# Kernel tuning notes

Measured on AMD Instinct MI355X. Metric: run time of the kernel, lower is better.

The kernel has to match this reference:

```python
import math
import jax, jax.numpy as jnp
import numpy as np

N = 512; E_EDGES = 16384; NODE_DIM = 64; HID = 128; FF = 2048; VOCAB = 50; L = 2; H = 8; SEQ = 100


def setup_inputs() -> dict:
    key = jax.random.key(0)
    ks = jax.random.split(key, 24)
    s = 0.02
    rn = lambda k, shape: jax.random.normal(k, shape, jnp.float32) * s
    return {
        "x": jax.random.normal(ks[0], (N, NODE_DIM), jnp.float32),
        "edge_index": jax.random.randint(ks[1], (2, E_EDGES), 0, N, dtype=jnp.int32),
        "gcn1_w": rn(ks[2], (NODE_DIM, HID)), "gcn1_b": rn(ks[3], (HID,)),
        "gcn2_w": rn(ks[4], (HID, HID)),     "gcn2_b": rn(ks[5], (HID,)),
        "fc_w":   rn(ks[6], (HID, HID)),     "fc_b":   rn(ks[7], (HID,)),
        # decoder: per layer, 4 proj mats (q,k,v,out) for self-attn and cross-attn
        "sa_w": rn(ks[8], (L, 4, HID, HID)), "sa_b": rn(ks[9], (L, 4, HID)),
        "ca_w": rn(ks[10], (L, 4, HID, HID)), "ca_b": rn(ks[11], (L, 4, HID)),
        "ln_w": jnp.ones((L, 3, HID), jnp.float32), "ln_b": jnp.zeros((L, 3, HID), jnp.float32),
        "ff_w1": rn(ks[12], (L, HID, FF)), "ff_b1": rn(ks[13], (L, FF)),
        "ff_w2": rn(ks[14], (L, FF, HID)), "ff_b2": rn(ks[15], (L, HID)),
        "out_w": rn(ks[16], (HID, VOCAB)), "out_b": rn(ks[17], (VOCAB,)),
    }


def _gcn(x, W, b, src, dst, n):
    # PyG GCNConv: add self-loops, symmetric norm, aggregate source->target
    h = x @ W                                   # [N, out]
    loop = jnp.arange(n, dtype=src.dtype)
    s = jnp.concatenate([src, loop])
    d = jnp.concatenate([dst, loop])
    deg = jax.ops.segment_sum(jnp.ones_like(d, x.dtype), d, num_segments=n)
    dinv = jax.lax.rsqrt(deg)                   # deg >= 1 thanks to self-loops
    norm = dinv[s] * dinv[d]                    # [E+N]
    return jax.ops.segment_sum(h[s] * norm[:, None], d, num_segments=n) + b


def _layernorm(x, w, b, eps=1e-5):
    m = x.mean(-1, keepdims=True)
    v = ((x - m) ** 2).mean(-1, keepdims=True)
    return (x - m) * jax.lax.rsqrt(v + eps) * w + b


def _mha(q_in, kv_in, w, b):
    # q_in [S,Nb,E], kv_in [T,Nb,E]; w [4,E,E] (q,k,v,out), b [4,E]
    S, Nb, E = q_in.shape
    T = kv_in.shape[0]
    Dh = E // H
    q = (q_in @ w[0] + b[0]).reshape(S, Nb, H, Dh)
    k = (kv_in @ w[1] + b[1]).reshape(T, Nb, H, Dh)
    v = (kv_in @ w[2] + b[2]).reshape(T, Nb, H, Dh)
    att = jnp.einsum('snhd,tnhd->nhst', q, k) / math.sqrt(Dh)
    p = jax.nn.softmax(att, axis=-1)
    o = jnp.einsum('nhst,tnhd->snhd', p, v).reshape(S, Nb, E)
    return o @ w[3] + b[3]


def _forward(x, edge_index, gcn1_w, gcn1_b, gcn2_w, gcn2_b, fc_w, fc_b,
             sa_w, sa_b, ca_w, ca_b, ln_w, ln_b, ff_w1, ff_b1, ff_w2, ff_b2,
             out_w, out_b):
    n = x.shape[0]
    src, dst = edge_index[0], edge_index[1]
    # quantum_embedding: rz = (cos(phi)-sin(phi)) * (cos(theta)*x + sin(theta)*tanh(x))
    qx = (math.cos(0.05) - math.sin(0.05)) * (math.cos(0.1) * x + math.sin(0.1) * jnp.tanh(x))
    h = jax.nn.relu(_gcn(qx, gcn1_w, gcn1_b, src, dst, n))
    h = jax.nn.relu(_gcn(h, gcn2_w, gcn2_b, src, dst, n))
    h = h @ fc_w + fc_b                          # [N, HID]
    mem = h[None]                                # [1, N, HID] (memory, seq-first)
    tgt = jnp.zeros((SEQ, n, h.shape[1]), h.dtype)
    for l in range(L):                           # post-norm TransformerDecoderLayer
        tgt = _layernorm(tgt + _mha(tgt, tgt, sa_w[l], sa_b[l]), ln_w[l, 0], ln_b[l, 0])
        tgt = _layernorm(tgt + _mha(tgt, mem, ca_w[l], ca_b[l]), ln_w[l, 1], ln_b[l, 1])
        f = jax.nn.relu(tgt @ ff_w1[l] + ff_b1[l]) @ ff_w2[l] + ff_b2[l]
        tgt = _layernorm(tgt + f, ln_w[l, 2], ln_b[l, 2])
    return tgt @ out_w + out_b                   # [SEQ, N, VOCAB]


def reference(x, edge_index, gcn1_w, gcn1_b, gcn2_w, gcn2_b, fc_w, fc_b,
              sa_w, sa_b, ca_w, ca_b, ln_w, ln_b, ff_w1, ff_b1, ff_w2, ff_b2,
              out_w, out_b):
    return _forward(x, edge_index, gcn1_w, gcn1_b, gcn2_w, gcn2_b, fc_w, fc_b,
                    sa_w, sa_b, ca_w, ca_b, ln_w, ln_b, ff_w1, ff_b1, ff_w2, ff_b2,
                    out_w, out_b)
```

## Files before the change

### kernel.cpp

```cpp
#include <hip/hip_runtime.h>
#include <math.h>

#define NN      512
#define EE      16384
#define NDIM    64
#define HID     128
#define FFD     2048
#define VOCAB   50
#define SEQ     100

#define QA 0.94877109112428797f
#define QB 0.99500416527802582f
#define QC 0.099833416646828155f

struct GArgs {
    const int* ei;
    const float* x; const float* g1w; const float* g1b;
    const float* g2w; const float* g2b;
    const float* fcw; const float* fcb;
    const float* saw; const float* sab;
    const float* caw; const float* cab;
    const float* lnw; const float* lnb;
    const float* fw1; const float* fb1; const float* fw2; const float* fb2;
    const float* ow; const float* ob;
    float* out;
    int* offs; int* csr;
    float* dinv; float* pre1; float* pre2; float* t2;
    float* Msa1; float* Mca0; float* Mca1; float* sa0bias;
};


__device__ __forceinline__ float gather_row(const float* __restrict__ pre,
                                            const float* __restrict__ dinv,
                                            const int* __restrict__ offs,
                                            const int* __restrict__ csr,
                                            int row, int j) {
    float dd = dinv[row];
    float acc = pre[row * HID + j] * dd;
    int i = offs[row], e = offs[row + 1];
    for (; i + 3 < e; i += 4) {
        int s0 = csr[i], s1 = csr[i + 1], s2 = csr[i + 2], s3 = csr[i + 3];
        float a0 = pre[s0 * HID + j] * dinv[s0];
        float a1 = pre[s1 * HID + j] * dinv[s1];
        float a2 = pre[s2 * HID + j] * dinv[s2];
        float a3 = pre[s3 * HID + j] * dinv[s3];
        acc += (a0 + a1) + (a2 + a3);
    }
    for (; i < e; ++i) {
        int s = csr[i];
        acc += pre[s * HID + j] * dinv[s];
    }
    return acc * dd;
}

__device__ __forceinline__ float rowln4(float v, float w, float b, float* sh, int t) {
    int r = t >> 7;
    float s1 = v, s2 = v * v;
#pragma unroll
    for (int o = 32; o > 0; o >>= 1) {
        s1 += __shfl_down(s1, o);
        s2 += __shfl_down(s2, o);
    }
    int wv = (t >> 6) & 1;
    if ((t & 63) == 0) { sh[r * 4 + wv] = s1; sh[r * 4 + 2 + wv] = s2; }
    __syncthreads();
    float mean = (sh[r * 4] + sh[r * 4 + 1]) * (1.0f / HID);
    float m2   = (sh[r * 4 + 2] + sh[r * 4 + 3]) * (1.0f / HID);
    float rstd = rsqrtf(m2 - mean * mean + 1e-5f);
    float out = (v - mean) * rstd * w + b;
    __syncthreads();
    return out;
}

__device__ __forceinline__ float ff_core(const float* __restrict__ W1,
                                         const float* __restrict__ b1,
                                         const float* __restrict__ W2,
                                         const float* sh_x, float* sh_m, int t) {
    {
        int c4 = t * 4;
        float4 bb = *(const float4*)&b1[c4];
        float a0x = bb.x, a0y = bb.y, a0z = bb.z, a0w = bb.w;
        float a1x = bb.x, a1y = bb.y, a1z = bb.z, a1w = bb.w;
        float a2x = bb.x, a2y = bb.y, a2z = bb.z, a2w = bb.w;
        float a3x = bb.x, a3y = bb.y, a3z = bb.z, a3w = bb.w;
        const float* w1p = W1 + c4;
#pragma unroll 4
        for (int k = 0; k < HID; k++) {
            float4 w = *(const float4*)&w1p[k * FFD];
            float s0 = sh_x[0 * HID + k], s1 = sh_x[1 * HID + k];
            float s2 = sh_x[2 * HID + k], s3 = sh_x[3 * HID + k];
            a0x = fmaf(s0, w.x, a0x); a0y = fmaf(s0, w.y, a0y);
            a0z = fmaf(s0, w.z, a0z); a0w = fmaf(s0, w.w, a0w);
            a1x = fmaf(s1, w.x, a1x); a1y = fmaf(s1, w.y, a1y);
            a1z = fmaf(s1, w.z, a1z); a1w = fmaf(s1, w.w, a1w);
            a2x = fmaf(s2, w.x, a2x); a2y = fmaf(s2, w.y, a2y);
            a2z = fmaf(s2, w.z, a2z); a2w = fmaf(s2, w.w, a2w);
            a3x = fmaf(s3, w.x, a3x); a3y = fmaf(s3, w.y, a3y);
            a3z = fmaf(s3, w.z, a3z); a3w = fmaf(s3, w.w, a3w);
        }
        float4 m;
        m.x = fmaxf(a0x, 0.f); m.y = fmaxf(a0y, 0.f); m.z = fmaxf(a0z, 0.f); m.w = fmaxf(a0w, 0.f);
        *(float4*)&sh_m[0 * FFD + c4] = m;
        m.x = fmaxf(a1x, 0.f); m.y = fmaxf(a1y, 0.f); m.z = fmaxf(a1z, 0.f); m.w = fmaxf(a1w, 0.f);
        *(float4*)&sh_m[1 * FFD + c4] = m;
        m.x = fmaxf(a2x, 0.f); m.y = fmaxf(a2y, 0.f); m.z = fmaxf(a2z, 0.f); m.w = fmaxf(a2w, 0.f);
        *(float4*)&sh_m[2 * FFD + c4] = m;
        m.x = fmaxf(a3x, 0.f); m.y = fmaxf(a3y, 0.f); m.z = fmaxf(a3z, 0.f); m.w = fmaxf(a3w, 0.f);
        *(float4*)&sh_m[3 * FFD + c4] = m;
    }
    __syncthreads();

    float4 p0 = {0, 0, 0, 0}, p1 = p0, p2 = p0, p3 = p0;
    {
        int col4 = (t & 31) * 4, k0 = (t >> 5) * 128;
        const float* w2p = W2 + col4;
#pragma unroll 8
        for (int kk = 0; kk < 128; kk++) {
            int k = k0 + kk;
            float4 w = *(const float4*)&w2p[k * HID];
            float m0 = sh_m[0 * FFD + k], m1 = sh_m[1 * FFD + k];
            float m2 = sh_m[2 * FFD + k], m3 = sh_m[3 * FFD + k];
            p0.x = fmaf(m0, w.x, p0.x); p0.y = fmaf(m0, w.y, p0.y);
            p0.z = fmaf(m0, w.z, p0.z); p0.w = fmaf(m0, w.w, p0.w);
            p1.x = fmaf(m1, w.x, p1.x); p1.y = fmaf(m1, w.y, p1.y);
            p1.z = fmaf(m1, w.z, p1.z); p1.w = fmaf(m1, w.w, p1.w);
            p2.x = fmaf(m2, w.x, p2.x); p2.y = fmaf(m2, w.y, p2.y);
            p2.z = fmaf(m2, w.z, p2.z); p2.w = fmaf(m2, w.w, p2.w);
            p3.x = fmaf(m3, w.x, p3.x); p3.y = fmaf(m3, w.y, p3.y);
            p3.z = fmaf(m3, w.z, p3.z); p3.w = fmaf(m3, w.w, p3.w);
        }
    }
    __syncthreads();
    {
        int col4 = (t & 31) * 4, kq = t >> 5;
        *(float4*)&sh_m[kq * 512 + 0 * 128 + col4] = p0;
        *(float4*)&sh_m[kq * 512 + 1 * 128 + col4] = p1;
        *(float4*)&sh_m[kq * 512 + 2 * 128 + col4] = p2;
        *(float4*)&sh_m[kq * 512 + 3 * 128 + col4] = p3;
    }
    __syncthreads();
    int j = t & 127, r = t >> 7;
    float v = 0.0f;
#pragma unroll
    for (int kq = 0; kq < 16; kq++) v += sh_m[kq * 512 + r * 128 + j];
    return v;
}


__global__ __launch_bounds__(512) void k_a(GArgs a) {
    __shared__ __align__(16) float smem[1024];
    int bid = blockIdx.x, t = threadIdx.x;
    if (bid == 0) {
        int* scnt = (int*)smem;
        int* scur = scnt + 512;
        scnt[t] = 0;
        __syncthreads();
#pragma unroll
        for (int i = 0; i < 32; i++) {
            int e = i * 512 + t;
            atomicAdd(&scnt[a.ei[EE + e]], 1);
        }
        __syncthreads();
        int c = scnt[t];
        int v = c;
        for (int o = 1; o < 512; o <<= 1) {
            int add = (t >= o) ? scnt[t - o] : 0;
            __syncthreads();
            v += add;
            scnt[t] = v;
            __syncthreads();
        }
        a.offs[t + 1] = v;
        if (t == 0) a.offs[0] = 0;
        scur[t] = v - c;
        a.dinv[t] = rsqrtf((float)c + 1.0f);
        __syncthreads();
#pragma unroll
        for (int i = 0; i < 32; i++) {
            int e = i * 512 + t;
            int d = a.ei[EE + e];
            int slot = atomicAdd(&scur[d], 1);
            a.csr[slot] = a.ei[e];
        }
    } else if (bid <= 64) {
        float* qxs = smem;
        int row0 = (bid - 1) * 8;
        float vx = a.x[row0 * NDIM + t];
        qxs[t] = QA * (QB * vx + QC * tanhf(vx));
        __syncthreads();
        int col = t & 127, r0 = t >> 7;
#pragma unroll
        for (int rr = 0; rr < 2; rr++) {
            int r = r0 + rr * 4;
            float acc = 0.0f;
#pragma unroll 8
            for (int k = 0; k < NDIM; k++)
                acc = fmaf(qxs[r * 64 + k], a.g1w[k * HID + col], acc);
            a.pre1[(row0 + r) * HID + col] = acc;
        }
    } else if (bid <= 163) {
        int q = bid - 65;
        int jm = q / 33;
        int i = (q - jm * 33) * 512 + t;
        if (i < 129 * HID) {
            const float* A  = (jm == 0) ? (a.saw + (4 + 2) * HID * HID)
                             : (jm == 1) ? (a.caw + 2 * HID * HID)
                                         : (a.caw + (4 + 2) * HID * HID);
            const float* ab = (jm == 0) ? (a.sab + (4 + 2) * HID)
                             : (jm == 1) ? (a.cab + 2 * HID)
                                         : (a.cab + (4 + 2) * HID);
            const float* Bm = (jm == 0) ? (a.saw + (4 + 3) * HID * HID)
                             : (jm == 1) ? (a.caw + 3 * HID * HID)
                                         : (a.caw + (4 + 3) * HID * HID);
            const float* bb = (jm == 0) ? (a.sab + (4 + 3) * HID)
                             : (jm == 1) ? (a.cab + 3 * HID)
                                         : (a.cab + (4 + 3) * HID);
            float* outM = (jm == 0) ? a.Msa1 : (jm == 1) ? a.Mca0 : a.Mca1;
            int rw = i >> 7, col = i & 127;
            float acc;
            if (rw < 128) {
                const float* ar = A + rw * HID;
                acc = 0.0f;
#pragma unroll 8
                for (int k = 0; k < HID; k++) acc = fmaf(ar[k], Bm[k * HID + col], acc);
            } else {
                acc = bb[col];
#pragma unroll 8
                for (int k = 0; k < HID; k++) acc = fmaf(ab[k], Bm[k * HID + col], acc);
            }
            outM[i] = acc;
        }
    } else {
        if (t < HID) {
            const float* ab3 = a.sab + 2 * HID;
            const float* B3  = a.saw + 3 * HID * HID;
            float acc = a.sab[3 * HID + t];
#pragma unroll 8
            for (int k = 0; k < HID; k++) acc = fmaf(ab3[k], B3[k * HID + t], acc);
            a.sa0bias[t] = acc;
        }
    }
}


__global__ __launch_bounds__(512) void k_b2(GArgs a) {
    __shared__ float sh_h[4 * HID];
    int t = threadIdx.x, j = t & 127, r = t >> 7;
    int row = blockIdx.x * 4 + r;
    float g = gather_row(a.pre1, a.dinv, a.offs, a.csr, row, j);
    sh_h[r * HID + j] = fmaxf(g + a.g1b[j], 0.0f);
    __syncthreads();
    float acc = 0.0f;
#pragma unroll 8
    for (int k = 0; k < HID; k++)
        acc = fmaf(sh_h[r * HID + k], a.g2w[k * HID + j], acc);
    a.pre2[row * HID + j] = acc;
}


__global__ __launch_bounds__(512) void k_ffA(GArgs a) {
    __shared__ __align__(16) float sh_x[4 * HID];
    __shared__ __align__(16) float sh_h[4 * HID];
    __shared__ __align__(16) float sh_ca[4 * HID];
    __shared__ __align__(16) float sh_m[4 * FFD];
    __shared__ float shln[16];
    int bid = blockIdx.x, t = threadIdx.x;
    int j = t & 127, r = t >> 7;
    int row = bid * 4 + r;

    float g = gather_row(a.pre2, a.dinv, a.offs, a.csr, row, j);
    sh_h[r * HID + j] = fmaxf(g + a.g2b[j], 0.0f);
    __syncthreads();
    float mv = a.fcb[j];
#pragma unroll 8
    for (int k = 0; k < HID; k++) mv = fmaf(sh_h[r * HID + k], a.fcw[k * HID + j], mv);
    __syncthreads();
    sh_h[r * HID + j] = mv;
    __syncthreads();
    float c0 = a.Mca0[128 * HID + j], c1 = a.Mca1[128 * HID + j];
#pragma unroll 4
    for (int k = 0; k < HID; k++) {
        float m = sh_h[r * HID + k];
        c0 = fmaf(m, a.Mca0[k * HID + j], c0);
        c1 = fmaf(m, a.Mca1[k * HID + j], c1);
    }
    sh_ca[r * HID + j] = c1;
    float v0 = rowln4(a.sa0bias[j], a.lnw[j], a.lnb[j], shln, t);
    v0 = rowln4(v0 + c0, a.lnw[HID + j], a.lnb[HID + j], shln, t);
    sh_x[r * HID + j] = v0;
    __syncthreads();

    float v = ff_core(a.fw1, a.fb1, a.fw2, sh_x, sh_m, t);

    v += a.fb2[j] + sh_x[r * HID + j];
    float t1 = rowln4(v, a.lnw[2 * HID + j], a.lnb[2 * HID + j], shln, t);
    __syncthreads();
    sh_h[r * HID + j] = t1;
    __syncthreads();
    float s1 = a.Msa1[128 * HID + j];
#pragma unroll 8
    for (int k = 0; k < HID; k++)
        s1 = fmaf(sh_h[r * HID + k], a.Msa1[k * HID + j], s1);
    float u = rowln4(t1 + s1, a.lnw[3 * HID + j], a.lnb[3 * HID + j], shln, t);
    u = rowln4(u + sh_ca[r * HID + j], a.lnw[4 * HID + j], a.lnb[4 * HID + j], shln, t);
    a.t2[row * HID + j] = u;
}


__global__ __launch_bounds__(512) void k_ffB(GArgs a) {
    __shared__ __align__(16) float sh_x[4 * HID];
    __shared__ __align__(16) float sh_h[4 * HID];
    __shared__ __align__(16) float sh_m[4 * FFD];
    __shared__ __align__(16) float sh_lg[4 * VOCAB];
    __shared__ float shln[16];
    int bid = blockIdx.x, t = threadIdx.x;
    int j = t & 127, r = t >> 7;

    if (t < 128) ((float4*)sh_x)[t] = ((const float4*)(a.t2 + bid * 4 * HID))[t];
    __syncthreads();

    float v = ff_core(a.fw1 + HID * FFD, a.fb1 + FFD, a.fw2 + FFD * HID, sh_x, sh_m, t);

    v += a.fb2[HID + j] + sh_x[r * HID + j];
    float w = rowln4(v, a.lnw[5 * HID + j], a.lnb[5 * HID + j], shln, t);
    __syncthreads();
    sh_h[r * HID + j] = w;
    __syncthreads();
    if (t < 4 * VOCAB) {
        int rr = t / VOCAB, c = t - rr * VOCAB;
        float acc = a.ob[c];
#pragma unroll 8
        for (int k = 0; k < HID; k++)
            acc = fmaf(sh_h[rr * HID + k], a.ow[k * VOCAB + c], acc);
        sh_lg[rr * VOCAB + c] = acc;
    }
    __syncthreads();
    const float4* lg4 = (const float4*)sh_lg;
    float4* out4 = (float4*)a.out;
    int base4 = bid * 50;
    for (int idx = t; idx < SEQ * 50; idx += 512) {
        int s = idx / 50, q = idx - s * 50;
        out4[s * (NN * VOCAB / 4) + base4 + q] = lg4[q];
    }
}


extern "C" void kernel_launch(void* const* d_in, const int* in_sizes, int n_in,
                              void* d_out, int out_size, void* d_ws, size_t ws_size,
                              hipStream_t stream) {
    (void)in_sizes; (void)n_in; (void)out_size; (void)ws_size;
    GArgs a;
    a.x   = (const float*)d_in[0];
    a.ei  = (const int*)d_in[1];
    a.g1w = (const float*)d_in[2];
    a.g1b = (const float*)d_in[3];
    a.g2w = (const float*)d_in[4];
    a.g2b = (const float*)d_in[5];
    a.fcw = (const float*)d_in[6];
    a.fcb = (const float*)d_in[7];
    a.saw = (const float*)d_in[8];
    a.sab = (const float*)d_in[9];
    a.caw = (const float*)d_in[10];
    a.cab = (const float*)d_in[11];
    a.lnw = (const float*)d_in[12];
    a.lnb = (const float*)d_in[13];
    a.fw1 = (const float*)d_in[14];
    a.fb1 = (const float*)d_in[15];
    a.fw2 = (const float*)d_in[16];
    a.fb2 = (const float*)d_in[17];
    a.ow  = (const float*)d_in[18];
    a.ob  = (const float*)d_in[19];
    a.out = (float*)d_out;

    float* ws = (float*)d_ws;
    a.pre1    = ws;
    a.pre2    = ws + 65536;
    a.t2      = ws + 131072;
    a.Msa1    = ws + 196608;
    a.Mca0    = ws + 213120;
    a.Mca1    = ws + 229632;
    a.sa0bias = ws + 246144;
    a.dinv    = ws + 246272;
    a.offs    = (int*)(ws + 246784);
    a.csr     = a.offs + 516;

    k_a  <<<165, 512, 0, stream>>>(a);
    k_b2 <<<128, 512, 0, stream>>>(a);
    k_ffA<<<128, 512, 0, stream>>>(a);
    k_ffB<<<128, 512, 0, stream>>>(a);
}
```

Before: 123.1 us.

## Split FF kernels to two rows per block and stagger weight reads

```diff
diff --git a/kernel.cpp b/kernel.cpp
--- a/kernel.cpp
+++ b/kernel.cpp
@@ -25,7 +25,7 @@
     const float* ow; const float* ob;
     float* out;
     int* offs; int* csr;
-    float* dinv; float* pre1; float* pre2; float* t2;
+    float* dinv; float* pre1; float* pre2; float* t0; float* ca1; float* t2;
     float* Msa1; float* Mca0; float* Mca1; float* sa0bias;
 };
 
@@ -72,77 +72,60 @@
     return out;
 }
 
-__device__ __forceinline__ float ff_core(const float* __restrict__ W1,
-                                         const float* __restrict__ b1,
-                                         const float* __restrict__ W2,
-                                         const float* sh_x, float* sh_m, int t) {
+__device__ __forceinline__ float ff2_core(const float* __restrict__ W1,
+                                          const float* __restrict__ b1,
+                                          const float* __restrict__ W2,
+                                          const float* sh_x, float* sh_m,
+                                          float* sh_p, int t, int koff) {
     {
         int c4 = t * 4;
         float4 bb = *(const float4*)&b1[c4];
         float a0x = bb.x, a0y = bb.y, a0z = bb.z, a0w = bb.w;
         float a1x = bb.x, a1y = bb.y, a1z = bb.z, a1w = bb.w;
-        float a2x = bb.x, a2y = bb.y, a2z = bb.z, a2w = bb.w;
-        float a3x = bb.x, a3y = bb.y, a3z = bb.z, a3w = bb.w;
         const float* w1p = W1 + c4;
-#pragma unroll 4
-        for (int k = 0; k < HID; k++) {
+#pragma unroll 8
+        for (int kk = 0; kk < HID; kk++) {
+            int k = (kk + koff) & (HID - 1);
             float4 w = *(const float4*)&w1p[k * FFD];
-            float s0 = sh_x[0 * HID + k], s1 = sh_x[1 * HID + k];
-            float s2 = sh_x[2 * HID + k], s3 = sh_x[3 * HID + k];
+            float s0 = sh_x[k], s1 = sh_x[HID + k];
             a0x = fmaf(s0, w.x, a0x); a0y = fmaf(s0, w.y, a0y);
             a0z = fmaf(s0, w.z, a0z); a0w = fmaf(s0, w.w, a0w);
             a1x = fmaf(s1, w.x, a1x); a1y = fmaf(s1, w.y, a1y);
             a1z = fmaf(s1, w.z, a1z); a1w = fmaf(s1, w.w, a1w);
-            a2x = fmaf(s2, w.x, a2x); a2y = fmaf(s2, w.y, a2y);
-            a2z = fmaf(s2, w.z, a2z); a2w = fmaf(s2, w.w, a2w);
-            a3x = fmaf(s3, w.x, a3x); a3y = fmaf(s3, w.y, a3y);
-            a3z = fmaf(s3, w.z, a3z); a3w = fmaf(s3, w.w, a3w);
         }
         float4 m;
-        m.x = fmaxf(a0x, 0.f); m.y = fmaxf(a0y, 0.f); m.z = fmaxf(a0z, 0.f); m.w = fmaxf(a0w, 0.f);
-        *(float4*)&sh_m[0 * FFD + c4] = m;
-        m.x = fmaxf(a1x, 0.f); m.y = fmaxf(a1y, 0.f); m.z = fmaxf(a1z, 0.f); m.w = fmaxf(a1w, 0.f);
-        *(float4*)&sh_m[1 * FFD + c4] = m;
-        m.x = fmaxf(a2x, 0.f); m.y = fmaxf(a2y, 0.f); m.z = fmaxf(a2z, 0.f); m.w = fmaxf(a2w, 0.f);
-        *(float4*)&sh_m[2 * FFD + c4] = m;
-        m.x = fmaxf(a3x, 0.f); m.y = fmaxf(a3y, 0.f); m.z = fmaxf(a3z, 0.f); m.w = fmaxf(a3w, 0.f);
-        *(float4*)&sh_m[3 * FFD + c4] = m;
-    }
-    __syncthreads();
-
-    float4 p0 = {0, 0, 0, 0}, p1 = p0, p2 = p0, p3 = p0;
+        m.x = fmaxf(a0x, 0.f); m.y = fmaxf(a0y, 0.f);
+        m.z = fmaxf(a0z, 0.f); m.w = fmaxf(a0w, 0.f);
+        *(float4*)&sh_m[c4] = m;
+        m.x = fmaxf(a1x, 0.f); m.y = fmaxf(a1y, 0.f);
+        m.z = fmaxf(a1z, 0.f); m.w = fmaxf(a1w, 0.f);
+        *(float4*)&sh_m[FFD + c4] = m;
+    }
+    __syncthreads();
+
     {
-        int col4 = (t & 31) * 4, k0 = (t >> 5) * 128;
+        int kq = t >> 5, col4 = (t & 31) * 4;
+        int k0 = kq * 128;
+        float4 p0 = {0, 0, 0, 0}, p1 = {0, 0, 0, 0};
         const float* w2p = W2 + col4;
 #pragma unroll 8
         for (int kk = 0; kk < 128; kk++) {
-            int k = k0 + kk;
+            int k = k0 + ((kk + koff) & 127);
             float4 w = *(const float4*)&w2p[k * HID];
-            float m0 = sh_m[0 * FFD + k], m1 = sh_m[1 * FFD + k];
-            float m2 = sh_m[2 * FFD + k], m3 = sh_m[3 * FFD + k];
+            float m0 = sh_m[k], m1 = sh_m[FFD + k];
             p0.x = fmaf(m0, w.x, p0.x); p0.y = fmaf(m0, w.y, p0.y);
             p0.z = fmaf(m0, w.z, p0.z); p0.w = fmaf(m0, w.w, p0.w);
             p1.x = fmaf(m1, w.x, p1.x); p1.y = fmaf(m1, w.y, p1.y);
             p1.z = fmaf(m1, w.z, p1.z); p1.w = fmaf(m1, w.w, p1.w);
-            p2.x = fmaf(m2, w.x, p2.x); p2.y = fmaf(m2, w.y, p2.y);
-            p2.z = fmaf(m2, w.z, p2.z); p2.w = fmaf(m2, w.w, p2.w);
-            p3.x = fmaf(m3, w.x, p3.x); p3.y = fmaf(m3, w.y, p3.y);
-            p3.z = fmaf(m3, w.z, p3.z); p3.w = fmaf(m3, w.w, p3.w);
-        }
-    }
-    __syncthreads();
-    {
-        int col4 = (t & 31) * 4, kq = t >> 5;
-        *(float4*)&sh_m[kq * 512 + 0 * 128 + col4] = p0;
-        *(float4*)&sh_m[kq * 512 + 1 * 128 + col4] = p1;
-        *(float4*)&sh_m[kq * 512 + 2 * 128 + col4] = p2;
-        *(float4*)&sh_m[kq * 512 + 3 * 128 + col4] = p3;
-    }
-    __syncthreads();
-    int j = t & 127, r = t >> 7;
+        }
+        *(float4*)&sh_p[kq * 256 + col4] = p0;
+        *(float4*)&sh_p[kq * 256 + 128 + col4] = p1;
+    }
+    __syncthreads();
+    int j = t & 127, r = (t >> 7) & 1;
     float v = 0.0f;
 #pragma unroll
-    for (int kq = 0; kq < 16; kq++) v += sh_m[kq * 512 + r * 128 + j];
+    for (int kq = 0; kq < 16; kq++) v += sh_p[kq * 256 + r * 128 + j];
     return v;
 }
 
@@ -258,16 +241,13 @@
 }
 
 
-__global__ __launch_bounds__(512) void k_ffA(GArgs a) {
-    __shared__ __align__(16) float sh_x[4 * HID];
-    __shared__ __align__(16) float sh_h[4 * HID];
-    __shared__ __align__(16) float sh_ca[4 * HID];
-    __shared__ __align__(16) float sh_m[4 * FFD];
-    __shared__ float shln[16];
-    int bid = blockIdx.x, t = threadIdx.x;
-    int j = t & 127, r = t >> 7;
-    int row = bid * 4 + r;
-
+__global__ __launch_bounds__(512) void k_c2(GArgs a) {
+    __shared__ __align__(16) float smem[1040];
+    float* sh_h = smem;
+    float* sh_m = smem + 512;
+    float* shln = smem + 1024;
+    int t = threadIdx.x, j = t & 127, r = t >> 7;
+    int row = blockIdx.x * 4 + r;
     float g = gather_row(a.pre2, a.dinv, a.offs, a.csr, row, j);
     sh_h[r * HID + j] = fmaxf(g + a.g2b[j], 0.0f);
     __syncthreads();
@@ -275,71 +255,85 @@
 #pragma unroll 8
     for (int k = 0; k < HID; k++) mv = fmaf(sh_h[r * HID + k], a.fcw[k * HID + j], mv);
     __syncthreads();
-    sh_h[r * HID + j] = mv;
+    sh_m[r * HID + j] = mv;
     __syncthreads();
     float c0 = a.Mca0[128 * HID + j], c1 = a.Mca1[128 * HID + j];
 #pragma unroll 4
     for (int k = 0; k < HID; k++) {
-        float m = sh_h[r * HID + k];
+        float m = sh_m[r * HID + k];
         c0 = fmaf(m, a.Mca0[k * HID + j], c0);
         c1 = fmaf(m, a.Mca1[k * HID + j], c1);
     }
-    sh_ca[r * HID + j] = c1;
-    float v0 = rowln4(a.sa0bias[j], a.lnw[j], a.lnb[j], shln, t);
-    v0 = rowln4(v0 + c0, a.lnw[HID + j], a.lnb[HID + j], shln, t);
-    sh_x[r * HID + j] = v0;
-    __syncthreads();
-
-    float v = ff_core(a.fw1, a.fb1, a.fw2, sh_x, sh_m, t);
-
-    v += a.fb2[j] + sh_x[r * HID + j];
-    float t1 = rowln4(v, a.lnw[2 * HID + j], a.lnb[2 * HID + j], shln, t);
-    __syncthreads();
-    sh_h[r * HID + j] = t1;
-    __syncthreads();
-    float s1 = a.Msa1[128 * HID + j];
-#pragma unroll 8
-    for (int k = 0; k < HID; k++)
-        s1 = fmaf(sh_h[r * HID + k], a.Msa1[k * HID + j], s1);
-    float u = rowln4(t1 + s1, a.lnw[3 * HID + j], a.lnb[3 * HID + j], shln, t);
-    u = rowln4(u + sh_ca[r * HID + j], a.lnw[4 * HID + j], a.lnb[4 * HID + j], shln, t);
-    a.t2[row * HID + j] = u;
-}
-
-
-__global__ __launch_bounds__(512) void k_ffB(GArgs a) {
-    __shared__ __align__(16) float sh_x[4 * HID];
-    __shared__ __align__(16) float sh_h[4 * HID];
-    __shared__ __align__(16) float sh_m[4 * FFD];
-    __shared__ __align__(16) float sh_lg[4 * VOCAB];
+    a.ca1[row * HID + j] = c1;
+    float v = rowln4(a.sa0bias[j], a.lnw[j], a.lnb[j], shln, t);
+    v = rowln4(v + c0, a.lnw[HID + j], a.lnb[HID + j], shln, t);
+    a.t0[row * HID + j] = v;
+}
+
+
+__global__ __launch_bounds__(512) void k_ffA(GArgs a) {
+    __shared__ __align__(16) float sh_x[2 * HID];
+    __shared__ __align__(16) float sh_s[2 * HID];
+    __shared__ __align__(16) float sh_m[2 * FFD];
+    __shared__ __align__(16) float sh_p[16 * 256];
     __shared__ float shln[16];
     int bid = blockIdx.x, t = threadIdx.x;
-    int j = t & 127, r = t >> 7;
-
-    if (t < 128) ((float4*)sh_x)[t] = ((const float4*)(a.t2 + bid * 4 * HID))[t];
-    __syncthreads();
-
-    float v = ff_core(a.fw1 + HID * FFD, a.fb1 + FFD, a.fw2 + FFD * HID, sh_x, sh_m, t);
-
-    v += a.fb2[HID + j] + sh_x[r * HID + j];
+    int row0 = bid * 2;
+    if (t < 64) ((float4*)sh_x)[t] = ((const float4*)(a.t0 + row0 * HID))[t];
+    __syncthreads();
+    int koff = (bid * 37) & 127;
+    float v = ff2_core(a.fw1, a.fb1, a.fw2, sh_x, sh_m, sh_p, t, koff);
+    int j = t & 127, rr = (t >> 7) & 1;
+    v += a.fb2[j] + sh_x[rr * HID + j];
+    float t1 = rowln4(v, a.lnw[2 * HID + j], a.lnb[2 * HID + j], shln, t);
+    __syncthreads();
+    sh_s[rr * HID + j] = t1;
+    __syncthreads();
+    float s1 = a.Msa1[128 * HID + j];
+#pragma unroll 8
+    for (int k = 0; k < HID; k++)
+        s1 = fmaf(sh_s[rr * HID + k], a.Msa1[k * HID + j], s1);
+    float u = rowln4(t1 + s1, a.lnw[3 * HID + j], a.lnb[3 * HID + j], shln, t);
+    u = rowln4(u + a.ca1[(row0 + rr) * HID + j],
+               a.lnw[4 * HID + j], a.lnb[4 * HID + j], shln, t);
+    if (t < 256) a.t2[(row0 + rr) * HID + j] = u;
+}
+
+
+__global__ __launch_bounds__(512) void k_ffB(GArgs a) {
+    __shared__ __align__(16) float sh_x[2 * HID];
+    __shared__ __align__(16) float sh_s[2 * HID];
+    __shared__ __align__(16) float sh_m[2 * FFD];
+    __shared__ __align__(16) float sh_p[16 * 256];
+    __shared__ __align__(16) float sh_lg[2 * VOCAB];
+    __shared__ float shln[16];
+    int bid = blockIdx.x, t = threadIdx.x;
+    int row0 = bid * 2;
+    if (t < 64) ((float4*)sh_x)[t] = ((const float4*)(a.t2 + row0 * HID))[t];
+    __syncthreads();
+    int koff = (bid * 37) & 127;
+    float v = ff2_core(a.fw1 + HID * FFD, a.fb1 + FFD, a.fw2 + FFD * HID,
+                       sh_x, sh_m, sh_p, t, koff);
+    int j = t & 127, rr = (t >> 7) & 1;
+    v += a.fb2[HID + j] + sh_x[rr * HID + j];
     float w = rowln4(v, a.lnw[5 * HID + j], a.lnb[5 * HID + j], shln, t);
     __syncthreads();
-    sh_h[r * HID + j] = w;
-    __syncthreads();
-    if (t < 4 * VOCAB) {
-        int rr = t / VOCAB, c = t - rr * VOCAB;
+    sh_s[rr * HID + j] = w;
+    __syncthreads();
+    if (t < 2 * VOCAB) {
+        int r2 = t / VOCAB, c = t - r2 * VOCAB;
         float acc = a.ob[c];
 #pragma unroll 8
         for (int k = 0; k < HID; k++)
-            acc = fmaf(sh_h[rr * HID + k], a.ow[k * VOCAB + c], acc);
-        sh_lg[rr * VOCAB + c] = acc;
+            acc = fmaf(sh_s[r2 * HID + k], a.ow[k * VOCAB + c], acc);
+        sh_lg[t] = acc;
     }
     __syncthreads();
     const float4* lg4 = (const float4*)sh_lg;
     float4* out4 = (float4*)a.out;
-    int base4 = bid * 50;
-    for (int idx = t; idx < SEQ * 50; idx += 512) {
-        int s = idx / 50, q = idx - s * 50;
+    int base4 = bid * 25;
+    for (int idx = t; idx < SEQ * 25; idx += 512) {
+        int s = idx / 25, q = idx - s * 25;
         out4[s * (NN * VOCAB / 4) + base4 + q] = lg4[q];
     }
 }
@@ -375,17 +369,20 @@
     float* ws = (float*)d_ws;
     a.pre1    = ws;
     a.pre2    = ws + 65536;
-    a.t2      = ws + 131072;
-    a.Msa1    = ws + 196608;
-    a.Mca0    = ws + 213120;
-    a.Mca1    = ws + 229632;
-    a.sa0bias = ws + 246144;
-    a.dinv    = ws + 246272;
-    a.offs    = (int*)(ws + 246784);
+    a.t0      = ws + 131072;
+    a.ca1     = ws + 196608;
+    a.t2      = ws + 262144;
+    a.Msa1    = ws + 327680;
+    a.Mca0    = ws + 344192;
+    a.Mca1    = ws + 360704;
+    a.sa0bias = ws + 377216;
+    a.dinv    = ws + 377344;
+    a.offs    = (int*)(ws + 377856);
     a.csr     = a.offs + 516;
 
     k_a  <<<165, 512, 0, stream>>>(a);
     k_b2 <<<128, 512, 0, stream>>>(a);
-    k_ffA<<<128, 512, 0, stream>>>(a);
-    k_ffB<<<128, 512, 0, stream>>>(a);
-}
+    k_c2 <<<128, 512, 0, stream>>>(a);
+    k_ffA<<<256, 512, 0, stream>>>(a);
+    k_ffB<<<256, 512, 0, stream>>>(a);
+}
```

Measured after the change: 114.5 us. 7.0% less time.
